# Optimization experiments

Hardware: AMD Instinct MI355X
Metric: run time of the kernel (lower is better)

Reference implementation:

```python
import jax, jax.numpy as jnp
import numpy as np

B, S, D_IN, E, H, F, O = 32, 1024, 256, 512, 512, 2048, 512


def setup_inputs() -> dict:
    key = jax.random.key(0)
    ks = jax.random.split(key, 10)
    s = 0.02
    return {
        "x": jax.random.normal(ks[0], (B, S, D_IN), dtype=jnp.float32),
        "W_enc": jax.random.normal(ks[1], (D_IN, E), dtype=jnp.float32) * s,
        "b_enc": jnp.zeros((E,), dtype=jnp.float32),
        "W_ih": jax.random.normal(ks[2], (E, 4 * H), dtype=jnp.float32) * s,
        "W_hh": jax.random.normal(ks[3], (H, 4 * H), dtype=jnp.float32) * s,
        "b_lstm": jnp.zeros((4 * H,), dtype=jnp.float32),
        "W1": jax.random.normal(ks[4], (E, F), dtype=jnp.float32) * s,
        "b1": jnp.zeros((F,), dtype=jnp.float32),
        "W2": jax.random.normal(ks[5], (F, O), dtype=jnp.float32) * s,
        "b2": jnp.zeros((O,), dtype=jnp.float32),
    }


def _lstm(xs, W_ih, W_hh, b):
    # xs: [S, B, E] -> outputs [S, B, H], final (h, c) each [B, H]
    h0 = jnp.zeros((xs.shape[1], W_hh.shape[0]), dtype=xs.dtype)
    c0 = jnp.zeros_like(h0)

    def step(carry, x_t):
        h, c = carry
        z = x_t @ W_ih + h @ W_hh + b  # [B, 4H]
        i, f, g, o = jnp.split(z, 4, axis=-1)
        i = jax.nn.sigmoid(i)
        f = jax.nn.sigmoid(f)
        g = jnp.tanh(g)
        o = jax.nn.sigmoid(o)
        c = f * c + i * g
        h = o * jnp.tanh(c)
        return (h, c), h

    (h_n, c_n), ys = jax.lax.scan(step, (h0, c0), xs)
    return ys, h_n, c_n


def reference(x, W_enc, b_enc, W_ih, W_hh, b_lstm, W1, b1, W2, b2):
    # encoder: per-token linear projection, then permute to time-major
    embedded = x @ W_enc + b_enc              # [B, S, E]
    embedded = jnp.transpose(embedded, (1, 0, 2))  # [S, B, E]
    # decoder LSTM over the sequence dimension
    output, h_n, c_n = _lstm(embedded, W_ih, W_hh, b_lstm)
    # per-position 2-layer MLP (vectorized version of the (i,j) loop):
    # fc2(fc1(relu(embedded)))  -- note ReLU is applied BEFORE fc1, and no
    # nonlinearity between fc1 and fc2, matching the torch code.
    embed_out = (jax.nn.relu(embedded) @ W1 + b1) @ W2 + b2  # [S, B, O]
    return output, h_n[None], c_n[None], embed_out
```

## Files before the change

### kernel.cpp

```cpp
#include <hip/hip_runtime.h>
#include <hip/hip_bf16.h>
#include <stdint.h>

typedef uint16_t u16;
typedef uint32_t u32;
typedef unsigned long long u64;
typedef __attribute__((ext_vector_type(8))) short short8;
typedef __attribute__((ext_vector_type(4))) float f32x4;

#define NS 1024

__device__ __forceinline__ float bf2f(u16 v) {
  union { u32 u; float f; } x; x.u = ((u32)v) << 16; return x.f;
}
__device__ __forceinline__ u16 f2bf(float f) {
  union { float f; u32 u; } x; x.f = f;
  u32 r = x.u + 0x7FFFu + ((x.u >> 16) & 1u);
  return (u16)(r >> 16);
}
__device__ __forceinline__ u32 relu2bf(u32 x) {
  u32 kill = (((x >> 15) & 1u) * 0x0000FFFFu) | (((x >> 31) & 1u) * 0xFFFF0000u);
  return x & ~kill;
}
__device__ __forceinline__ f32x4 shfl_x4(f32x4 v, int m) {
  f32x4 r;
  r[0] = __shfl_xor(v[0], m); r[1] = __shfl_xor(v[1], m);
  r[2] = __shfl_xor(v[2], m); r[3] = __shfl_xor(v[3], m);
  return r;
}
__device__ __forceinline__ float fsig(float x) {
  return 1.f / (1.f + __expf(-x));
}
__device__ __forceinline__ float ftanh(float x) {
  float t = __expf(2.f * x);
  return 1.f - 2.f / (t + 1.f);
}

__global__ __launch_bounds__(256) void k_cast(const float* __restrict__ in,
                                              u16* __restrict__ out, int n4) {
  int i = blockIdx.x * 256 + threadIdx.x;
  if (i >= n4) return;
  float4 v = ((const float4*)in)[i];
  ushort4 o;
  o.x = f2bf(v.x); o.y = f2bf(v.y); o.z = f2bf(v.z); o.w = f2bf(v.w);
  ((ushort4*)out)[i] = o;
}

__global__ __launch_bounds__(256) void k_transpose(const float* __restrict__ in,
                                                   u16* __restrict__ out,
                                                   int K, int N) {
  __shared__ u16 tile[32][33];
  int k0 = blockIdx.x * 32, n0 = blockIdx.y * 32;
  int tid = threadIdx.x;
#pragma unroll
  for (int i = 0; i < 4; i++) {
    int idx = i * 256 + tid;
    int r = idx >> 5, c = idx & 31;
    tile[r][c] = f2bf(in[(size_t)(k0 + r) * N + n0 + c]);
  }
  __syncthreads();
#pragma unroll
  for (int i = 0; i < 4; i++) {
    int idx = i * 256 + tid;
    int r = idx >> 5, c = idx & 31;
    out[(size_t)(n0 + r) * K + k0 + c] = tile[c][r];
  }
}

template <bool REMAP, bool RELU_A, bool OUTF32>
__global__ __launch_bounds__(256) void k_gemm(const u16* __restrict__ A,
                                              const u16* __restrict__ Bt,
                                              const float* __restrict__ bias,
                                              void* __restrict__ Cout,
                                              int M, int N, int K) {
  __shared__ u16 As[128 * 32];
  __shared__ u16 Bs[128 * 32];
  const int m0 = blockIdx.x * 128, n0 = blockIdx.y * 128;
  const int tid = threadIdx.x;
  const int wave = tid >> 6, lane = tid & 63;
  const int wm = wave >> 1, wn = wave & 1;
  f32x4 acc[4][4] = {};

  for (int kt = 0; kt < K; kt += 32) {
    uint4 av[2], bv[2];
#pragma unroll
    for (int i = 0; i < 2; i++) {
      int idx = i * 256 + tid;
      int r = idx >> 2, ch = idx & 3;
      av[i] = *(const uint4*)(A + (size_t)(m0 + r) * K + kt + ch * 8);
      bv[i] = *(const uint4*)(Bt + (size_t)(n0 + r) * K + kt + ch * 8);
      if (RELU_A) {
        u32* p = (u32*)&av[i];
        p[0] = relu2bf(p[0]); p[1] = relu2bf(p[1]);
        p[2] = relu2bf(p[2]); p[3] = relu2bf(p[3]);
      }
    }
    __syncthreads();
#pragma unroll
    for (int i = 0; i < 2; i++) {
      int idx = i * 256 + tid;
      int r = idx >> 2, ch = idx & 3;
      *(uint4*)(As + r * 32 + ch * 8) = av[i];
      *(uint4*)(Bs + r * 32 + ch * 8) = bv[i];
    }
    __syncthreads();
    short8 af[4], bf[4];
#pragma unroll
    for (int mi = 0; mi < 4; mi++) {
      int row = wm * 64 + mi * 16 + (lane & 15);
      af[mi] = *(const short8*)(As + row * 32 + (lane >> 4) * 8);
    }
#pragma unroll
    for (int ni = 0; ni < 4; ni++) {
      int col = wn * 64 + ni * 16 + (lane & 15);
      bf[ni] = *(const short8*)(Bs + col * 32 + (lane >> 4) * 8);
    }
#pragma unroll
    for (int mi = 0; mi < 4; mi++)
#pragma unroll
      for (int ni = 0; ni < 4; ni++)
        acc[mi][ni] = __builtin_amdgcn_mfma_f32_16x16x32_bf16(af[mi], bf[ni], acc[mi][ni], 0, 0, 0);
  }

#pragma unroll
  for (int mi = 0; mi < 4; mi++)
#pragma unroll
    for (int ni = 0; ni < 4; ni++) {
      int col = n0 + wn * 64 + ni * 16 + (lane & 15);
      float bvad = bias[col];
#pragma unroll
      for (int r = 0; r < 4; r++) {
        int row = m0 + wm * 64 + mi * 16 + (lane >> 4) * 4 + r;
        float v = acc[mi][ni][r] + bvad;
        size_t orow = REMAP ? ((size_t)(row & 1023) * 32 + (size_t)(row >> 10))
                            : (size_t)row;
        if (OUTF32) ((float*)Cout)[orow * N + col] = v;
        else        ((u16*)Cout)[orow * N + col] = f2bf(v);
      }
    }
}

__global__ __launch_bounds__(256, 1) void k_lstm(
    const u16* __restrict__ Whh_t,
    const u16* __restrict__ Wih_t,
    const u16* __restrict__ emb,
    const float* __restrict__ b_lstm,
    u64* __restrict__ hbuf,
    float* __restrict__ out,
    float* __restrict__ hn,
    float* __restrict__ cn)
{
  __shared__ u16 hl[2][32][512];

  const int blk = blockIdx.x;
  const int tid = threadIdx.x;
  const int wave = tid >> 6, lane = tid & 63;
  const int hc0 = blk * 8;
  const int mt = wave >> 1, nt = wave & 1;
  const int g = (lane >> 2) & 3;
  const int j = lane & 3;
  const int arow = mt * 16 + (lane & 15);
  const int crow0 = mt * 16 + (lane >> 4) * 4;
  const int mycol = hc0 + nt * 4 + j;
  const int srow = tid >> 3;
  const int st8 = tid & 7;

  short8 bfh[16], bfx[16];
  {
    int lc = lane & 15;
    int gcol = (lc >> 2) * 512 + hc0 + nt * 4 + (lc & 3);
    const u16* bh = Whh_t + (size_t)gcol * 512 + (lane >> 4) * 8;
    const u16* bx = Wih_t + (size_t)gcol * 512 + (lane >> 4) * 8;
#pragma unroll
    for (int kc = 0; kc < 16; kc++) {
      bfh[kc] = *(const short8*)(bh + kc * 32);
      bfx[kc] = *(const short8*)(bx + kc * 32);
    }
  }
  const float bz = b_lstm[g * 512 + hc0 + nt * 4 + j];

  f32x4 cst = {0.f, 0.f, 0.f, 0.f}, hst = {0.f, 0.f, 0.f, 0.f};

  f32x4 zx0 = {0.f, 0.f, 0.f, 0.f}, zx1 = {0.f, 0.f, 0.f, 0.f};
  {
    const u16* xb = emb + (size_t)arow * 512 + (lane >> 4) * 8;
    short8 af[16];
#pragma unroll
    for (int kc = 0; kc < 16; kc++) af[kc] = *(const short8*)(xb + kc * 32);
#pragma unroll
    for (int kc = 0; kc < 16; kc += 2) {
      zx0 = __builtin_amdgcn_mfma_f32_16x16x32_bf16(af[kc], bfx[kc], zx0, 0, 0, 0);
      zx1 = __builtin_amdgcn_mfma_f32_16x16x32_bf16(af[kc + 1], bfx[kc + 1], zx1, 0, 0, 0);
    }
  }

  char* ldsb = (char*)&hl[0][0][0];

#pragma unroll 1
  for (int s = 0; s < NS; s++) {
    {
      const u64* base = hbuf + (size_t)(s & 1) * 8192 + (size_t)srow * 256;
      const u32 want = (u32)s;
      u32 d[32];
      u32 miss = 0;
#pragma unroll
      for (int k = 0; k < 8; k++)
#pragma unroll
        for (int m = 0; m < 4; m++) {
          int i = k * 4 + m;
          int p = (k * 8 + st8) * 4 + m;
          u64 q = __hip_atomic_load(base + p, __ATOMIC_RELAXED, __HIP_MEMORY_SCOPE_AGENT);
          d[i] = (u32)q;
          if ((u32)(q >> 32) != want) miss |= (1u << i);
        }
      while (__any(miss != 0u)) {
        __builtin_amdgcn_s_sleep(1);
#pragma unroll
        for (int k = 0; k < 8; k++)
#pragma unroll
          for (int m = 0; m < 4; m++) {
            int i = k * 4 + m;
            if (miss & (1u << i)) {
              int p = (k * 8 + st8) * 4 + m;
              u64 q = __hip_atomic_load(base + p, __ATOMIC_RELAXED, __HIP_MEMORY_SCOPE_AGENT);
              if ((u32)(q >> 32) == want) { d[i] = (u32)q; miss &= ~(1u << i); }
            }
          }
      }
      char* lw = ldsb + (size_t)(s & 1) * 32768 + (size_t)srow * 1024;
#pragma unroll
      for (int k = 0; k < 8; k++) {
        uint4 v;
        v.x = d[k * 4]; v.y = d[k * 4 + 1]; v.z = d[k * 4 + 2]; v.w = d[k * 4 + 3];
        int slot = k * 8 + st8;
        int sw = (slot & ~7) | ((slot ^ srow) & 7);
        *(uint4*)(lw + sw * 16) = v;
      }
    }
    __syncthreads();

    f32x4 a0 = zx0, a1 = zx1;
    {
      const char* lr = ldsb + (size_t)(s & 1) * 32768 + (size_t)arow * 1024;
#pragma unroll
      for (int kc = 0; kc < 16; kc += 2) {
        int sl0 = kc * 4 + (lane >> 4);
        int sw0 = (sl0 & ~7) | ((sl0 ^ arow) & 7);
        short8 fa = *(const short8*)(lr + sw0 * 16);
        int sl1 = sl0 + 4;
        int sw1 = (sl1 & ~7) | ((sl1 ^ arow) & 7);
        short8 fb = *(const short8*)(lr + sw1 * 16);
        a0 = __builtin_amdgcn_mfma_f32_16x16x32_bf16(fa, bfh[kc], a0, 0, 0, 0);
        a1 = __builtin_amdgcn_mfma_f32_16x16x32_bf16(fb, bfh[kc + 1], a1, 0, 0, 0);
      }
    }

    f32x4 z0;
#pragma unroll
    for (int r = 0; r < 4; r++) z0[r] = a0[r] + a1[r] + bz;
    f32x4 z1 = shfl_x4(z0, 4);
    f32x4 z2 = shfl_x4(z0, 8);
    f32x4 z3 = shfl_x4(z1, 8);
    f32x4 zi_ = (g == 0) ? z0 : (g == 1) ? z1 : (g == 2) ? z2 : z3;
    f32x4 zf_ = (g == 0) ? z1 : (g == 1) ? z0 : (g == 2) ? z3 : z2;
    f32x4 zg_ = (g == 0) ? z2 : (g == 1) ? z3 : (g == 2) ? z0 : z1;
    f32x4 zo_ = (g == 0) ? z3 : (g == 1) ? z2 : (g == 2) ? z1 : z0;
#pragma unroll
    for (int r = 0; r < 4; r++) {
      float ig = fsig(zi_[r]);
      float fg = fsig(zf_[r]);
      float gg = ftanh(zg_[r]);
      float og = fsig(zo_[r]);
      cst[r] = fg * cst[r] + ig * gg;
      hst[r] = og * ftanh(cst[r]);
    }

    {
      u32 pair[4];
#pragma unroll
      for (int r = 0; r < 4; r++) {
        u16 hb = f2bf(hst[r]);
        u32 nb = (u32)(u16)__shfl_xor((int)hb, 1);
        pair[r] = (u32)hb | (nb << 16);
      }
      if (((lane & 15) & 13) == 0) {
        u64* dst = hbuf + (size_t)((s + 1) & 1) * 8192 + (size_t)crow0 * 256
                 + (size_t)(blk * 4 + nt * 2 + (j >> 1));
        u64 tag = ((u64)(u32)(s + 1)) << 32;
#pragma unroll
        for (int r = 0; r < 4; r++)
          __hip_atomic_store(dst + (size_t)r * 256, tag | pair[r],
                             __ATOMIC_RELAXED, __HIP_MEMORY_SCOPE_AGENT);
      }
    }

    if (g == 0) {
#pragma unroll
      for (int r = 0; r < 4; r++)
        out[((size_t)s * 32 + crow0 + r) * 512 + mycol] = hst[r];
    }

    if (s + 1 < NS) {
      const u16* xb = emb + ((size_t)(s + 1) * 32 + arow) * 512 + (lane >> 4) * 8;
      short8 af2[16];
#pragma unroll
      for (int kc = 0; kc < 16; kc++) af2[kc] = *(const short8*)(xb + kc * 32);
      f32x4 t0 = {0.f, 0.f, 0.f, 0.f}, t1 = {0.f, 0.f, 0.f, 0.f};
#pragma unroll
      for (int kc = 0; kc < 16; kc += 2) {
        t0 = __builtin_amdgcn_mfma_f32_16x16x32_bf16(af2[kc], bfx[kc], t0, 0, 0, 0);
        t1 = __builtin_amdgcn_mfma_f32_16x16x32_bf16(af2[kc + 1], bfx[kc + 1], t1, 0, 0, 0);
      }
      zx0 = t0; zx1 = t1;
    }
  }

  if (g == 0) {
#pragma unroll
    for (int r = 0; r < 4; r++) {
      hn[(size_t)(crow0 + r) * 512 + mycol] = hst[r];
      cn[(size_t)(crow0 + r) * 512 + mycol] = cst[r];
    }
  }
}

extern "C" void kernel_launch(void* const* d_in, const int* in_sizes, int n_in,
                              void* d_out, int out_size, void* d_ws, size_t ws_size,
                              hipStream_t stream) {
  (void)in_sizes; (void)n_in; (void)out_size; (void)ws_size;
  const float* x      = (const float*)d_in[0];
  const float* W_enc  = (const float*)d_in[1];
  const float* b_enc  = (const float*)d_in[2];
  const float* W_ih   = (const float*)d_in[3];
  const float* W_hh   = (const float*)d_in[4];
  const float* b_lstm = (const float*)d_in[5];
  const float* W1     = (const float*)d_in[6];
  const float* b1     = (const float*)d_in[7];
  const float* W2     = (const float*)d_in[8];
  const float* b2     = (const float*)d_in[9];

  char* ws = (char*)d_ws;
  size_t off = 0;
  auto alloc = [&](size_t bytes) -> void* {
    void* p = ws + off;
    off += (bytes + 255) & ~(size_t)255;
    return p;
  };
  u64* hbuf   = (u64*)alloc((size_t)2 * 32 * 256 * 8);
  u16* Wenc_t = (u16*)alloc((size_t)512 * 256 * 2);
  u16* Wih_t  = (u16*)alloc((size_t)2048 * 512 * 2);
  u16* Whh_t  = (u16*)alloc((size_t)2048 * 512 * 2);
  u16* W1_t   = (u16*)alloc((size_t)2048 * 512 * 2);
  u16* W2_t   = (u16*)alloc((size_t)512 * 2048 * 2);
  u16* big    = (u16*)alloc((size_t)8192 * 2048 * 2);
  u16* xbf    = big;
  u16* T      = big;

  float* outp = (float*)d_out;
  float* hnp  = outp + (size_t)16777216;
  float* cnp  = hnp + 16384;
  float* eop  = cnp + 16384;
  u16* emb  = (u16*)(eop + 8388608);

  hipMemsetAsync(hbuf, 0, (size_t)2 * 32 * 256 * 8, stream);

  k_cast<<<8192, 256, 0, stream>>>(x, xbf, 2097152);
  k_transpose<<<dim3(8, 16), 256, 0, stream>>>(W_enc, Wenc_t, 256, 512);
  k_transpose<<<dim3(16, 64), 256, 0, stream>>>(W_ih, Wih_t, 512, 2048);
  k_transpose<<<dim3(16, 64), 256, 0, stream>>>(W_hh, Whh_t, 512, 2048);
  k_transpose<<<dim3(16, 64), 256, 0, stream>>>(W1, W1_t, 512, 2048);
  k_transpose<<<dim3(64, 16), 256, 0, stream>>>(W2, W2_t, 2048, 512);

  k_gemm<true, false, false><<<dim3(256, 4), 256, 0, stream>>>(
      xbf, Wenc_t, b_enc, emb, 32768, 512, 256);

  {
    void* args[] = {(void*)&Whh_t, (void*)&Wih_t, (void*)&emb, (void*)&b_lstm,
                    (void*)&hbuf, (void*)&outp, (void*)&hnp, (void*)&cnp};
    hipError_t cerr = hipLaunchCooperativeKernel((const void*)k_lstm, dim3(64),
                                                 dim3(256), args, 0, stream);
    if (cerr != hipSuccess) {
      (void)hipGetLastError();
      k_lstm<<<dim3(64), dim3(256), 0, stream>>>(Whh_t, Wih_t, emb, b_lstm,
                                                 hbuf, outp, hnp, cnp);
    }
  }

  for (int cch = 0; cch < 4; cch++) {
    const u16* embc = emb + (size_t)cch * 8192 * 512;
    float* eoc = eop + (size_t)cch * 8192 * 512;
    k_gemm<false, true, false><<<dim3(64, 16), 256, 0, stream>>>(
        embc, W1_t, b1, T, 8192, 2048, 512);
    k_gemm<false, false, true><<<dim3(64, 4), 256, 0, stream>>>(
        T, W2_t, b2, eoc, 8192, 512, 2048);
  }
}
```

Before: 6.552 ms.

## Replace tagged per-element h exchange with flag-based block barrier and direct loads

The cross-block hidden-state exchange no longer tags every 64-bit word with a step counter. Each block now writes plain bf16 h values, then publishes a per-block sentinel with a release fence. Consumers spin on all 64 sentinels, issue an acquire fence, and read the MFMA A-fragments straight from global memory, so the LDS staging and swizzle are gone. This halves the exchange traffic and removes per-element polling, but adds a block-wide __syncthreads and a fence round trip on every step of the serial recurrence.

```diff
diff --git a/kernel.cpp b/kernel.cpp
--- a/kernel.cpp
+++ b/kernel.cpp
@@ -145,13 +145,12 @@
     const u16* __restrict__ Wih_t,
     const u16* __restrict__ emb,
     const float* __restrict__ b_lstm,
-    u64* __restrict__ hbuf,
+    u16* __restrict__ hbuf,
+    u32* __restrict__ sent,
     float* __restrict__ out,
     float* __restrict__ hn,
     float* __restrict__ cn)
 {
-  __shared__ u16 hl[2][32][512];
-
   const int blk = blockIdx.x;
   const int tid = threadIdx.x;
   const int wave = tid >> 6, lane = tid & 63;
@@ -162,8 +161,6 @@
   const int arow = mt * 16 + (lane & 15);
   const int crow0 = mt * 16 + (lane >> 4) * 4;
   const int mycol = hc0 + nt * 4 + j;
-  const int srow = tid >> 3;
-  const int st8 = tid & 7;
 
   short8 bfh[16], bfx[16];
   {
@@ -194,65 +191,28 @@
     }
   }
 
-  char* ldsb = (char*)&hl[0][0][0];
-
 #pragma unroll 1
   for (int s = 0; s < NS; s++) {
     {
-      const u64* base = hbuf + (size_t)(s & 1) * 8192 + (size_t)srow * 256;
-      const u32 want = (u32)s;
-      u32 d[32];
-      u32 miss = 0;
-#pragma unroll
-      for (int k = 0; k < 8; k++)
-#pragma unroll
-        for (int m = 0; m < 4; m++) {
-          int i = k * 4 + m;
-          int p = (k * 8 + st8) * 4 + m;
-          u64 q = __hip_atomic_load(base + p, __ATOMIC_RELAXED, __HIP_MEMORY_SCOPE_AGENT);
-          d[i] = (u32)q;
-          if ((u32)(q >> 32) != want) miss |= (1u << i);
-        }
-      while (__any(miss != 0u)) {
+      const u32* sp = sent + (size_t)lane * 32;
+      while (true) {
+        u32 v = __hip_atomic_load(sp, __ATOMIC_RELAXED, __HIP_MEMORY_SCOPE_AGENT);
+        if (__all(v >= (u32)s)) break;
         __builtin_amdgcn_s_sleep(1);
-#pragma unroll
-        for (int k = 0; k < 8; k++)
-#pragma unroll
-          for (int m = 0; m < 4; m++) {
-            int i = k * 4 + m;
-            if (miss & (1u << i)) {
-              int p = (k * 8 + st8) * 4 + m;
-              u64 q = __hip_atomic_load(base + p, __ATOMIC_RELAXED, __HIP_MEMORY_SCOPE_AGENT);
-              if ((u32)(q >> 32) == want) { d[i] = (u32)q; miss &= ~(1u << i); }
-            }
-          }
-      }
-      char* lw = ldsb + (size_t)(s & 1) * 32768 + (size_t)srow * 1024;
-#pragma unroll
-      for (int k = 0; k < 8; k++) {
-        uint4 v;
-        v.x = d[k * 4]; v.y = d[k * 4 + 1]; v.z = d[k * 4 + 2]; v.w = d[k * 4 + 3];
-        int slot = k * 8 + st8;
-        int sw = (slot & ~7) | ((slot ^ srow) & 7);
-        *(uint4*)(lw + sw * 16) = v;
-      }
-    }
-    __syncthreads();
+      }
+      __builtin_amdgcn_fence(__ATOMIC_ACQUIRE, "agent");
+    }
+
+    const u16* hb = hbuf + (size_t)(s & 1) * 16384 + (size_t)arow * 512 + (lane >> 4) * 8;
+    short8 hfr[16];
+#pragma unroll
+    for (int kc = 0; kc < 16; kc++) hfr[kc] = *(const short8*)(hb + kc * 32);
 
     f32x4 a0 = zx0, a1 = zx1;
-    {
-      const char* lr = ldsb + (size_t)(s & 1) * 32768 + (size_t)arow * 1024;
-#pragma unroll
-      for (int kc = 0; kc < 16; kc += 2) {
-        int sl0 = kc * 4 + (lane >> 4);
-        int sw0 = (sl0 & ~7) | ((sl0 ^ arow) & 7);
-        short8 fa = *(const short8*)(lr + sw0 * 16);
-        int sl1 = sl0 + 4;
-        int sw1 = (sl1 & ~7) | ((sl1 ^ arow) & 7);
-        short8 fb = *(const short8*)(lr + sw1 * 16);
-        a0 = __builtin_amdgcn_mfma_f32_16x16x32_bf16(fa, bfh[kc], a0, 0, 0, 0);
-        a1 = __builtin_amdgcn_mfma_f32_16x16x32_bf16(fb, bfh[kc + 1], a1, 0, 0, 0);
-      }
+#pragma unroll
+    for (int kc = 0; kc < 16; kc += 2) {
+      a0 = __builtin_amdgcn_mfma_f32_16x16x32_bf16(hfr[kc], bfh[kc], a0, 0, 0, 0);
+      a1 = __builtin_amdgcn_mfma_f32_16x16x32_bf16(hfr[kc + 1], bfh[kc + 1], a1, 0, 0, 0);
     }
 
     f32x4 z0;
@@ -279,19 +239,24 @@
       u32 pair[4];
 #pragma unroll
       for (int r = 0; r < 4; r++) {
-        u16 hb = f2bf(hst[r]);
-        u32 nb = (u32)(u16)__shfl_xor((int)hb, 1);
-        pair[r] = (u32)hb | (nb << 16);
+        u16 hb2 = f2bf(hst[r]);
+        u32 nb = (u32)(u16)__shfl_xor((int)hb2, 1);
+        pair[r] = (u32)hb2 | (nb << 16);
       }
       if (((lane & 15) & 13) == 0) {
-        u64* dst = hbuf + (size_t)((s + 1) & 1) * 8192 + (size_t)crow0 * 256
-                 + (size_t)(blk * 4 + nt * 2 + (j >> 1));
-        u64 tag = ((u64)(u32)(s + 1)) << 32;
-#pragma unroll
-        for (int r = 0; r < 4; r++)
-          __hip_atomic_store(dst + (size_t)r * 256, tag | pair[r],
-                             __ATOMIC_RELAXED, __HIP_MEMORY_SCOPE_AGENT);
-      }
+        u32* dst = (u32*)(hbuf + (size_t)((s + 1) & 1) * 16384
+                          + (size_t)crow0 * 512 + mycol);
+#pragma unroll
+        for (int r = 0; r < 4; r++) dst[(size_t)r * 256] = pair[r];
+      }
+    }
+
+    __syncthreads();
+    if (wave == 0) {
+      __builtin_amdgcn_fence(__ATOMIC_RELEASE, "agent");
+      if (lane == 0)
+        __hip_atomic_store(sent + (size_t)blk * 32, (u32)(s + 1),
+                           __ATOMIC_RELAXED, __HIP_MEMORY_SCOPE_AGENT);
     }
 
     if (g == 0) {
@@ -346,7 +311,8 @@
     off += (bytes + 255) & ~(size_t)255;
     return p;
   };
-  u64* hbuf   = (u64*)alloc((size_t)2 * 32 * 256 * 8);
+  u16* hbuf   = (u16*)alloc((size_t)2 * 32 * 512 * 2);
+  u32* sent   = (u32*)alloc((size_t)64 * 128);
   u16* Wenc_t = (u16*)alloc((size_t)512 * 256 * 2);
   u16* Wih_t  = (u16*)alloc((size_t)2048 * 512 * 2);
   u16* Whh_t  = (u16*)alloc((size_t)2048 * 512 * 2);
@@ -362,7 +328,7 @@
   float* eop  = cnp + 16384;
   u16* emb  = (u16*)(eop + 8388608);
 
-  hipMemsetAsync(hbuf, 0, (size_t)2 * 32 * 256 * 8, stream);
+  hipMemsetAsync(ws, 0, (size_t)2 * 32 * 512 * 2 + (size_t)64 * 128, stream);
 
   k_cast<<<8192, 256, 0, stream>>>(x, xbf, 2097152);
   k_transpose<<<dim3(8, 16), 256, 0, stream>>>(W_enc, Wenc_t, 256, 512);
@@ -376,13 +342,13 @@
 
   {
     void* args[] = {(void*)&Whh_t, (void*)&Wih_t, (void*)&emb, (void*)&b_lstm,
-                    (void*)&hbuf, (void*)&outp, (void*)&hnp, (void*)&cnp};
+                    (void*)&hbuf, (void*)&sent, (void*)&outp, (void*)&hnp, (void*)&cnp};
     hipError_t cerr = hipLaunchCooperativeKernel((const void*)k_lstm, dim3(64),
                                                  dim3(256), args, 0, stream);
     if (cerr != hipSuccess) {
       (void)hipGetLastError();
       k_lstm<<<dim3(64), dim3(256), 0, stream>>>(Whh_t, Wih_t, emb, b_lstm,
-                                                 hbuf, outp, hnp, cnp);
+                                                 hbuf, sent, outp, hnp, cnp);
     }
   }
 
```

After: 9.498 ms. 45.0% more time.

## Overlap MLP with LSTM in one cooperative kernel and fuse input cast into encoder GEMM

Applied to the files above, without the earlier changes.

Launches 256 blocks in one persistent kernel. The first 64 run the sequential LSTM recurrence and the remaining 192 compute the fused fc1→fc2 MLP per 16-row group, keeping the intermediate in LDS, so MLP work fills otherwise idle CUs during the latency-bound recurrence. The separate fp32→bf16 cast kernel is removed by converting x inside the encoder GEMM's A load, and the large intermediate buffer disappears. The risks are that MLP blocks compete with LSTM blocks for memory bandwidth and L2, which could slow the critical recurrence. The simple per-wave MFMA MLP also has much less data reuse than the tiled GEMM.

```diff
diff --git a/kernel.cpp b/kernel.cpp
--- a/kernel.cpp
+++ b/kernel.cpp
@@ -34,16 +34,6 @@
 __device__ __forceinline__ float ftanh(float x) {
   float t = __expf(2.f * x);
   return 1.f - 2.f / (t + 1.f);
-}
-
-__global__ __launch_bounds__(256) void k_cast(const float* __restrict__ in,
-                                              u16* __restrict__ out, int n4) {
-  int i = blockIdx.x * 256 + threadIdx.x;
-  if (i >= n4) return;
-  float4 v = ((const float4*)in)[i];
-  ushort4 o;
-  o.x = f2bf(v.x); o.y = f2bf(v.y); o.z = f2bf(v.z); o.w = f2bf(v.w);
-  ((ushort4*)out)[i] = o;
 }
 
 __global__ __launch_bounds__(256) void k_transpose(const float* __restrict__ in,
@@ -67,8 +57,8 @@
   }
 }
 
-template <bool REMAP, bool RELU_A, bool OUTF32>
-__global__ __launch_bounds__(256) void k_gemm(const u16* __restrict__ A,
+template <bool REMAP, bool RELU_A, bool OUTF32, bool A_F32>
+__global__ __launch_bounds__(256) void k_gemm(const void* __restrict__ Av,
                                               const u16* __restrict__ Bt,
                                               const float* __restrict__ bias,
                                               void* __restrict__ Cout,
@@ -87,7 +77,18 @@
     for (int i = 0; i < 2; i++) {
       int idx = i * 256 + tid;
       int r = idx >> 2, ch = idx & 3;
-      av[i] = *(const uint4*)(A + (size_t)(m0 + r) * K + kt + ch * 8);
+      if (A_F32) {
+        const float* Af = (const float*)Av;
+        const float* p = Af + (size_t)(m0 + r) * K + kt + ch * 8;
+        float4 f0 = *(const float4*)p;
+        float4 f1 = *(const float4*)(p + 4);
+        av[i].x = (u32)f2bf(f0.x) | ((u32)f2bf(f0.y) << 16);
+        av[i].y = (u32)f2bf(f0.z) | ((u32)f2bf(f0.w) << 16);
+        av[i].z = (u32)f2bf(f1.x) | ((u32)f2bf(f1.y) << 16);
+        av[i].w = (u32)f2bf(f1.z) | ((u32)f2bf(f1.w) << 16);
+      } else {
+        av[i] = *(const uint4*)((const u16*)Av + (size_t)(m0 + r) * K + kt + ch * 8);
+      }
       bv[i] = *(const uint4*)(Bt + (size_t)(n0 + r) * K + kt + ch * 8);
       if (RELU_A) {
         u32* p = (u32*)&av[i];
@@ -140,7 +141,7 @@
     }
 }
 
-__global__ __launch_bounds__(256, 1) void k_lstm(
+__global__ __launch_bounds__(256, 1) void k_main(
     const u16* __restrict__ Whh_t,
     const u16* __restrict__ Wih_t,
     const u16* __restrict__ emb,
@@ -148,178 +149,248 @@
     u64* __restrict__ hbuf,
     float* __restrict__ out,
     float* __restrict__ hn,
-    float* __restrict__ cn)
+    float* __restrict__ cn,
+    const u16* __restrict__ W1t,
+    const u16* __restrict__ W2t,
+    const float* __restrict__ b1,
+    const float* __restrict__ b2,
+    float* __restrict__ eop)
 {
-  __shared__ u16 hl[2][32][512];
+  __shared__ u16 smem[2 * 32 * 512];
 
   const int blk = blockIdx.x;
   const int tid = threadIdx.x;
-  const int wave = tid >> 6, lane = tid & 63;
-  const int hc0 = blk * 8;
-  const int mt = wave >> 1, nt = wave & 1;
-  const int g = (lane >> 2) & 3;
-  const int j = lane & 3;
-  const int arow = mt * 16 + (lane & 15);
-  const int crow0 = mt * 16 + (lane >> 4) * 4;
-  const int mycol = hc0 + nt * 4 + j;
-  const int srow = tid >> 3;
-  const int st8 = tid & 7;
-
-  short8 bfh[16], bfx[16];
-  {
-    int lc = lane & 15;
-    int gcol = (lc >> 2) * 512 + hc0 + nt * 4 + (lc & 3);
-    const u16* bh = Whh_t + (size_t)gcol * 512 + (lane >> 4) * 8;
-    const u16* bx = Wih_t + (size_t)gcol * 512 + (lane >> 4) * 8;
-#pragma unroll
-    for (int kc = 0; kc < 16; kc++) {
-      bfh[kc] = *(const short8*)(bh + kc * 32);
-      bfx[kc] = *(const short8*)(bx + kc * 32);
-    }
-  }
-  const float bz = b_lstm[g * 512 + hc0 + nt * 4 + j];
-
-  f32x4 cst = {0.f, 0.f, 0.f, 0.f}, hst = {0.f, 0.f, 0.f, 0.f};
-
-  f32x4 zx0 = {0.f, 0.f, 0.f, 0.f}, zx1 = {0.f, 0.f, 0.f, 0.f};
-  {
-    const u16* xb = emb + (size_t)arow * 512 + (lane >> 4) * 8;
-    short8 af[16];
-#pragma unroll
-    for (int kc = 0; kc < 16; kc++) af[kc] = *(const short8*)(xb + kc * 32);
-#pragma unroll
-    for (int kc = 0; kc < 16; kc += 2) {
-      zx0 = __builtin_amdgcn_mfma_f32_16x16x32_bf16(af[kc], bfx[kc], zx0, 0, 0, 0);
-      zx1 = __builtin_amdgcn_mfma_f32_16x16x32_bf16(af[kc + 1], bfx[kc + 1], zx1, 0, 0, 0);
-    }
-  }
-
-  char* ldsb = (char*)&hl[0][0][0];
+  const int lane = tid & 63;
+
+  if (blk < 64) {
+    const int wave = tid >> 6;
+    const int hc0 = blk * 8;
+    const int mt = wave >> 1, nt = wave & 1;
+    const int g = (lane >> 2) & 3;
+    const int j = lane & 3;
+    const int arow = mt * 16 + (lane & 15);
+    const int crow0 = mt * 16 + (lane >> 4) * 4;
+    const int mycol = hc0 + nt * 4 + j;
+    const int srow = tid >> 3;
+    const int st8 = tid & 7;
+
+    short8 bfh[16], bfx[16];
+    {
+      int lc = lane & 15;
+      int gcol = (lc >> 2) * 512 + hc0 + nt * 4 + (lc & 3);
+      const u16* bh = Whh_t + (size_t)gcol * 512 + (lane >> 4) * 8;
+      const u16* bx = Wih_t + (size_t)gcol * 512 + (lane >> 4) * 8;
+#pragma unroll
+      for (int kc = 0; kc < 16; kc++) {
+        bfh[kc] = *(const short8*)(bh + kc * 32);
+        bfx[kc] = *(const short8*)(bx + kc * 32);
+      }
+    }
+    const float bz = b_lstm[g * 512 + hc0 + nt * 4 + j];
+
+    f32x4 cst = {0.f, 0.f, 0.f, 0.f}, hst = {0.f, 0.f, 0.f, 0.f};
+
+    f32x4 zx0 = {0.f, 0.f, 0.f, 0.f}, zx1 = {0.f, 0.f, 0.f, 0.f};
+    {
+      const u16* xb = emb + (size_t)arow * 512 + (lane >> 4) * 8;
+      short8 af[16];
+#pragma unroll
+      for (int kc = 0; kc < 16; kc++) af[kc] = *(const short8*)(xb + kc * 32);
+#pragma unroll
+      for (int kc = 0; kc < 16; kc += 2) {
+        zx0 = __builtin_amdgcn_mfma_f32_16x16x32_bf16(af[kc], bfx[kc], zx0, 0, 0, 0);
+        zx1 = __builtin_amdgcn_mfma_f32_16x16x32_bf16(af[kc + 1], bfx[kc + 1], zx1, 0, 0, 0);
+      }
+    }
+
+    char* ldsb = (char*)smem;
 
 #pragma unroll 1
-  for (int s = 0; s < NS; s++) {
-    {
-      const u64* base = hbuf + (size_t)(s & 1) * 8192 + (size_t)srow * 256;
-      const u32 want = (u32)s;
-      u32 d[32];
-      u32 miss = 0;
-#pragma unroll
-      for (int k = 0; k < 8; k++)
-#pragma unroll
-        for (int m = 0; m < 4; m++) {
-          int i = k * 4 + m;
-          int p = (k * 8 + st8) * 4 + m;
-          u64 q = __hip_atomic_load(base + p, __ATOMIC_RELAXED, __HIP_MEMORY_SCOPE_AGENT);
-          d[i] = (u32)q;
-          if ((u32)(q >> 32) != want) miss |= (1u << i);
-        }
-      while (__any(miss != 0u)) {
-        __builtin_amdgcn_s_sleep(1);
+    for (int s = 0; s < NS; s++) {
+      {
+        const u64* base = hbuf + (size_t)(s & 1) * 8192 + (size_t)srow * 256;
+        const u32 want = (u32)s;
+        u32 d[32];
+        u32 miss = 0;
 #pragma unroll
         for (int k = 0; k < 8; k++)
 #pragma unroll
           for (int m = 0; m < 4; m++) {
             int i = k * 4 + m;
-            if (miss & (1u << i)) {
-              int p = (k * 8 + st8) * 4 + m;
-              u64 q = __hip_atomic_load(base + p, __ATOMIC_RELAXED, __HIP_MEMORY_SCOPE_AGENT);
-              if ((u32)(q >> 32) == want) { d[i] = (u32)q; miss &= ~(1u << i); }
+            int p = (k * 8 + st8) * 4 + m;
+            u64 q = __hip_atomic_load(base + p, __ATOMIC_RELAXED, __HIP_MEMORY_SCOPE_AGENT);
+            d[i] = (u32)q;
+            if ((u32)(q >> 32) != want) miss |= (1u << i);
+          }
+        while (__any(miss != 0u)) {
+          __builtin_amdgcn_s_sleep(1);
+#pragma unroll
+          for (int k = 0; k < 8; k++)
+#pragma unroll
+            for (int m = 0; m < 4; m++) {
+              int i = k * 4 + m;
+              if (miss & (1u << i)) {
+                int p = (k * 8 + st8) * 4 + m;
+                u64 q = __hip_atomic_load(base + p, __ATOMIC_RELAXED, __HIP_MEMORY_SCOPE_AGENT);
+                if ((u32)(q >> 32) == want) { d[i] = (u32)q; miss &= ~(1u << i); }
+              }
             }
-          }
-      }
-      char* lw = ldsb + (size_t)(s & 1) * 32768 + (size_t)srow * 1024;
-#pragma unroll
-      for (int k = 0; k < 8; k++) {
-        uint4 v;
-        v.x = d[k * 4]; v.y = d[k * 4 + 1]; v.z = d[k * 4 + 2]; v.w = d[k * 4 + 3];
-        int slot = k * 8 + st8;
-        int sw = (slot & ~7) | ((slot ^ srow) & 7);
-        *(uint4*)(lw + sw * 16) = v;
-      }
-    }
-    __syncthreads();
-
-    f32x4 a0 = zx0, a1 = zx1;
-    {
-      const char* lr = ldsb + (size_t)(s & 1) * 32768 + (size_t)arow * 1024;
-#pragma unroll
-      for (int kc = 0; kc < 16; kc += 2) {
-        int sl0 = kc * 4 + (lane >> 4);
-        int sw0 = (sl0 & ~7) | ((sl0 ^ arow) & 7);
-        short8 fa = *(const short8*)(lr + sw0 * 16);
-        int sl1 = sl0 + 4;
-        int sw1 = (sl1 & ~7) | ((sl1 ^ arow) & 7);
-        short8 fb = *(const short8*)(lr + sw1 * 16);
-        a0 = __builtin_amdgcn_mfma_f32_16x16x32_bf16(fa, bfh[kc], a0, 0, 0, 0);
-        a1 = __builtin_amdgcn_mfma_f32_16x16x32_bf16(fb, bfh[kc + 1], a1, 0, 0, 0);
-      }
-    }
-
-    f32x4 z0;
-#pragma unroll
-    for (int r = 0; r < 4; r++) z0[r] = a0[r] + a1[r] + bz;
-    f32x4 z1 = shfl_x4(z0, 4);
-    f32x4 z2 = shfl_x4(z0, 8);
-    f32x4 z3 = shfl_x4(z1, 8);
-    f32x4 zi_ = (g == 0) ? z0 : (g == 1) ? z1 : (g == 2) ? z2 : z3;
-    f32x4 zf_ = (g == 0) ? z1 : (g == 1) ? z0 : (g == 2) ? z3 : z2;
-    f32x4 zg_ = (g == 0) ? z2 : (g == 1) ? z3 : (g == 2) ? z0 : z1;
-    f32x4 zo_ = (g == 0) ? z3 : (g == 1) ? z2 : (g == 2) ? z1 : z0;
-#pragma unroll
-    for (int r = 0; r < 4; r++) {
-      float ig = fsig(zi_[r]);
-      float fg = fsig(zf_[r]);
-      float gg = ftanh(zg_[r]);
-      float og = fsig(zo_[r]);
-      cst[r] = fg * cst[r] + ig * gg;
-      hst[r] = og * ftanh(cst[r]);
-    }
-
-    {
-      u32 pair[4];
+        }
+        char* lw = ldsb + (size_t)(s & 1) * 32768 + (size_t)srow * 1024;
+#pragma unroll
+        for (int k = 0; k < 8; k++) {
+          uint4 v;
+          v.x = d[k * 4]; v.y = d[k * 4 + 1]; v.z = d[k * 4 + 2]; v.w = d[k * 4 + 3];
+          int slot = k * 8 + st8;
+          int sw = (slot & ~7) | ((slot ^ srow) & 7);
+          *(uint4*)(lw + sw * 16) = v;
+        }
+      }
+      __syncthreads();
+
+      f32x4 a0 = zx0, a1 = zx1;
+      {
+        const char* lr = ldsb + (size_t)(s & 1) * 32768 + (size_t)arow * 1024;
+#pragma unroll
+        for (int kc = 0; kc < 16; kc += 2) {
+          int sl0 = kc * 4 + (lane >> 4);
+          int sw0 = (sl0 & ~7) | ((sl0 ^ arow) & 7);
+          short8 fa = *(const short8*)(lr + sw0 * 16);
+          int sl1 = sl0 + 4;
+          int sw1 = (sl1 & ~7) | ((sl1 ^ arow) & 7);
+          short8 fb = *(const short8*)(lr + sw1 * 16);
+          a0 = __builtin_amdgcn_mfma_f32_16x16x32_bf16(fa, bfh[kc], a0, 0, 0, 0);
+          a1 = __builtin_amdgcn_mfma_f32_16x16x32_bf16(fb, bfh[kc + 1], a1, 0, 0, 0);
+        }
+      }
+
+      f32x4 z0;
+#pragma unroll
+      for (int r = 0; r < 4; r++) z0[r] = a0[r] + a1[r] + bz;
+      f32x4 z1 = shfl_x4(z0, 4);
+      f32x4 z2 = shfl_x4(z0, 8);
+      f32x4 z3 = shfl_x4(z1, 8);
+      f32x4 zi_ = (g == 0) ? z0 : (g == 1) ? z1 : (g == 2) ? z2 : z3;
+      f32x4 zf_ = (g == 0) ? z1 : (g == 1) ? z0 : (g == 2) ? z3 : z2;
+      f32x4 zg_ = (g == 0) ? z2 : (g == 1) ? z3 : (g == 2) ? z0 : z1;
+      f32x4 zo_ = (g == 0) ? z3 : (g == 1) ? z2 : (g == 2) ? z1 : z0;
 #pragma unroll
       for (int r = 0; r < 4; r++) {
-        u16 hb = f2bf(hst[r]);
-        u32 nb = (u32)(u16)__shfl_xor((int)hb, 1);
-        pair[r] = (u32)hb | (nb << 16);
-      }
-      if (((lane & 15) & 13) == 0) {
-        u64* dst = hbuf + (size_t)((s + 1) & 1) * 8192 + (size_t)crow0 * 256
-                 + (size_t)(blk * 4 + nt * 2 + (j >> 1));
-        u64 tag = ((u64)(u32)(s + 1)) << 32;
+        float ig = fsig(zi_[r]);
+        float fg = fsig(zf_[r]);
+        float gg = ftanh(zg_[r]);
+        float og = fsig(zo_[r]);
+        cst[r] = fg * cst[r] + ig * gg;
+        hst[r] = og * ftanh(cst[r]);
+      }
+
+      {
+        u32 pair[4];
+#pragma unroll
+        for (int r = 0; r < 4; r++) {
+          u16 hb = f2bf(hst[r]);
+          u32 nb = (u32)(u16)__shfl_xor((int)hb, 1);
+          pair[r] = (u32)hb | (nb << 16);
+        }
+        if (((lane & 15) & 13) == 0) {
+          u64* dst = hbuf + (size_t)((s + 1) & 1) * 8192 + (size_t)crow0 * 256
+                   + (size_t)(blk * 4 + nt * 2 + (j >> 1));
+          u64 tag = ((u64)(u32)(s + 1)) << 32;
+#pragma unroll
+          for (int r = 0; r < 4; r++)
+            __hip_atomic_store(dst + (size_t)r * 256, tag | pair[r],
+                               __ATOMIC_RELAXED, __HIP_MEMORY_SCOPE_AGENT);
+        }
+      }
+
+      if (g == 0) {
 #pragma unroll
         for (int r = 0; r < 4; r++)
-          __hip_atomic_store(dst + (size_t)r * 256, tag | pair[r],
-                             __ATOMIC_RELAXED, __HIP_MEMORY_SCOPE_AGENT);
+          out[((size_t)s * 32 + crow0 + r) * 512 + mycol] = hst[r];
+      }
+
+      if (s + 1 < NS) {
+        const u16* xb = emb + ((size_t)(s + 1) * 32 + arow) * 512 + (lane >> 4) * 8;
+        short8 af2[16];
+#pragma unroll
+        for (int kc = 0; kc < 16; kc++) af2[kc] = *(const short8*)(xb + kc * 32);
+        f32x4 t0 = {0.f, 0.f, 0.f, 0.f}, t1 = {0.f, 0.f, 0.f, 0.f};
+#pragma unroll
+        for (int kc = 0; kc < 16; kc += 2) {
+          t0 = __builtin_amdgcn_mfma_f32_16x16x32_bf16(af2[kc], bfx[kc], t0, 0, 0, 0);
+          t1 = __builtin_amdgcn_mfma_f32_16x16x32_bf16(af2[kc + 1], bfx[kc + 1], t1, 0, 0, 0);
+        }
+        zx0 = t0; zx1 = t1;
       }
     }
 
     if (g == 0) {
 #pragma unroll
-      for (int r = 0; r < 4; r++)
-        out[((size_t)s * 32 + crow0 + r) * 512 + mycol] = hst[r];
-    }
-
-    if (s + 1 < NS) {
-      const u16* xb = emb + ((size_t)(s + 1) * 32 + arow) * 512 + (lane >> 4) * 8;
-      short8 af2[16];
-#pragma unroll
-      for (int kc = 0; kc < 16; kc++) af2[kc] = *(const short8*)(xb + kc * 32);
-      f32x4 t0 = {0.f, 0.f, 0.f, 0.f}, t1 = {0.f, 0.f, 0.f, 0.f};
-#pragma unroll
-      for (int kc = 0; kc < 16; kc += 2) {
-        t0 = __builtin_amdgcn_mfma_f32_16x16x32_bf16(af2[kc], bfx[kc], t0, 0, 0, 0);
-        t1 = __builtin_amdgcn_mfma_f32_16x16x32_bf16(af2[kc + 1], bfx[kc + 1], t1, 0, 0, 0);
-      }
-      zx0 = t0; zx1 = t1;
-    }
-  }
-
-  if (g == 0) {
-#pragma unroll
-    for (int r = 0; r < 4; r++) {
-      hn[(size_t)(crow0 + r) * 512 + mycol] = hst[r];
-      cn[(size_t)(crow0 + r) * 512 + mycol] = cst[r];
+      for (int r = 0; r < 4; r++) {
+        hn[(size_t)(crow0 + r) * 512 + mycol] = hst[r];
+        cn[(size_t)(crow0 + r) * 512 + mycol] = cst[r];
+      }
+    }
+  } else {
+    const int mlpb = blk - 64;
+    const int wv = tid >> 6;
+    u16* T = smem;
+
+#pragma unroll 1
+    for (int grp = mlpb; grp < 2048; grp += 192) {
+      const int r0 = grp * 16;
+      __syncthreads();
+
+      short8 af[16];
+      {
+        const u16* ab = emb + (size_t)(r0 + (lane & 15)) * 512 + (lane >> 4) * 8;
+#pragma unroll
+        for (int kc = 0; kc < 16; kc++) {
+          short8 v = *(const short8*)(ab + kc * 32);
+          u32* p = (u32*)&v;
+          p[0] = relu2bf(p[0]); p[1] = relu2bf(p[1]);
+          p[2] = relu2bf(p[2]); p[3] = relu2bf(p[3]);
+          af[kc] = v;
+        }
+      }
+#pragma unroll 1
+      for (int ct = wv * 32; ct < wv * 32 + 32; ct++) {
+        const int col = ct * 16 + (lane & 15);
+        const u16* bb = W1t + (size_t)col * 512 + (lane >> 4) * 8;
+        f32x4 acc = {0.f, 0.f, 0.f, 0.f};
+#pragma unroll
+        for (int kc = 0; kc < 16; kc++) {
+          short8 bv = *(const short8*)(bb + kc * 32);
+          acc = __builtin_amdgcn_mfma_f32_16x16x32_bf16(af[kc], bv, acc, 0, 0, 0);
+        }
+        float bias = b1[col];
+#pragma unroll
+        for (int r = 0; r < 4; r++) {
+          int row = (lane >> 4) * 4 + r;
+          T[row * 2048 + col] = f2bf(acc[r] + bias);
+        }
+      }
+      __syncthreads();
+
+#pragma unroll 1
+      for (int ct = wv * 8; ct < wv * 8 + 8; ct++) {
+        const int col = ct * 16 + (lane & 15);
+        const u16* bb = W2t + (size_t)col * 2048 + (lane >> 4) * 8;
+        const u16* ta = T + (size_t)(lane & 15) * 2048 + (lane >> 4) * 8;
+        f32x4 acc = {0.f, 0.f, 0.f, 0.f};
+#pragma unroll
+        for (int kc = 0; kc < 64; kc++) {
+          short8 avv = *(const short8*)(ta + kc * 32);
+          short8 bvv = *(const short8*)(bb + kc * 32);
+          acc = __builtin_amdgcn_mfma_f32_16x16x32_bf16(avv, bvv, acc, 0, 0, 0);
+        }
+        float bias = b2[col];
+#pragma unroll
+        for (int r = 0; r < 4; r++) {
+          int row = (lane >> 4) * 4 + r;
+          eop[(size_t)(r0 + row) * 512 + col] = acc[r] + bias;
+        }
+      }
     }
   }
 }
@@ -352,46 +423,36 @@
   u16* Whh_t  = (u16*)alloc((size_t)2048 * 512 * 2);
   u16* W1_t   = (u16*)alloc((size_t)2048 * 512 * 2);
   u16* W2_t   = (u16*)alloc((size_t)512 * 2048 * 2);
-  u16* big    = (u16*)alloc((size_t)8192 * 2048 * 2);
-  u16* xbf    = big;
-  u16* T      = big;
+  u16* emb    = (u16*)alloc((size_t)32768 * 512 * 2);
 
   float* outp = (float*)d_out;
   float* hnp  = outp + (size_t)16777216;
   float* cnp  = hnp + 16384;
   float* eop  = cnp + 16384;
-  u16* emb  = (u16*)(eop + 8388608);
 
   hipMemsetAsync(hbuf, 0, (size_t)2 * 32 * 256 * 8, stream);
 
-  k_cast<<<8192, 256, 0, stream>>>(x, xbf, 2097152);
   k_transpose<<<dim3(8, 16), 256, 0, stream>>>(W_enc, Wenc_t, 256, 512);
   k_transpose<<<dim3(16, 64), 256, 0, stream>>>(W_ih, Wih_t, 512, 2048);
   k_transpose<<<dim3(16, 64), 256, 0, stream>>>(W_hh, Whh_t, 512, 2048);
   k_transpose<<<dim3(16, 64), 256, 0, stream>>>(W1, W1_t, 512, 2048);
   k_transpose<<<dim3(64, 16), 256, 0, stream>>>(W2, W2_t, 2048, 512);
 
-  k_gemm<true, false, false><<<dim3(256, 4), 256, 0, stream>>>(
-      xbf, Wenc_t, b_enc, emb, 32768, 512, 256);
+  k_gemm<true, false, false, true><<<dim3(256, 4), 256, 0, stream>>>(
+      x, Wenc_t, b_enc, emb, 32768, 512, 256);
 
   {
     void* args[] = {(void*)&Whh_t, (void*)&Wih_t, (void*)&emb, (void*)&b_lstm,
-                    (void*)&hbuf, (void*)&outp, (void*)&hnp, (void*)&cnp};
-    hipError_t cerr = hipLaunchCooperativeKernel((const void*)k_lstm, dim3(64),
+                    (void*)&hbuf, (void*)&outp, (void*)&hnp, (void*)&cnp,
+                    (void*)&W1_t, (void*)&W2_t, (void*)&b1, (void*)&b2,
+                    (void*)&eop};
+    hipError_t cerr = hipLaunchCooperativeKernel((const void*)k_main, dim3(256),
                                                  dim3(256), args, 0, stream);
     if (cerr != hipSuccess) {
       (void)hipGetLastError();
-      k_lstm<<<dim3(64), dim3(256), 0, stream>>>(Whh_t, Wih_t, emb, b_lstm,
-                                                 hbuf, outp, hnp, cnp);
+      k_main<<<dim3(256), dim3(256), 0, stream>>>(Whh_t, Wih_t, emb, b_lstm,
+                                                  hbuf, outp, hnp, cnp,
+                                                  W1_t, W2_t, b1, b2, eop);
     }
   }
-
-  for (int cch = 0; cch < 4; cch++) {
-    const u16* embc = emb + (size_t)cch * 8192 * 512;
-    float* eoc = eop + (size_t)cch * 8192 * 512;
-    k_gemm<false, true, false><<<dim3(64, 16), 256, 0, stream>>>(
-        embc, W1_t, b1, T, 8192, 2048, 512);
-    k_gemm<false, false, true><<<dim3(64, 4), 256, 0, stream>>>(
-        T, W2_t, b2, eoc, 8192, 512, 2048);
-  }
-}
+}
```

New measurement: 5.832 ms. 11.0% less time.
